# Performance work log

Measured on AMD Instinct MI355X. Metric: run time of the kernel, lower is better.

Reference implementation:

```python
import jax, jax.numpy as jnp
import numpy as np
from jax import lax

# Static config (matches init_kwargs)
DIM = 256; DR = 4; GROUP = 2; NH = 4; KS = 3; NA = 1; NUM_CLASS = 80; MUL = 5.0
CR = DIM // DR            # reduced dim = 64
GC = CR // GROUP          # offset-group channels = 32
HC = CR // NH             # per-head dim = 16
SCALE = HC ** -0.5
B, H, W = 8, 64, 64


def setup_inputs() -> dict:
    key = jax.random.key(0)
    ks_ = jax.random.split(key, 8)
    x = jax.random.normal(ks_[0], (B, DIM, H, W), jnp.float32)
    # offset = absolute pixel coordinates of the base sampling grid
    offset = jax.random.uniform(ks_[1], (B, NA * 2 * KS * KS, H, W), jnp.float32) * (H - 1)
    return dict(
        x=x, offset=offset,
        ln1_g=jnp.ones((DIM,), jnp.float32), ln1_b=jnp.zeros((DIM,), jnp.float32),
        w_qkv=jax.random.normal(ks_[2], (3 * CR, DIM), jnp.float32) * 0.02,
        w_dw=jax.random.normal(ks_[3], (GC, 1, 3, 3), jnp.float32) * 0.1,
        ln2_g=jnp.ones((GC,), jnp.float32), ln2_b=jnp.zeros((GC,), jnp.float32),
        w_off=jax.random.normal(ks_[4], (NA * 2 * KS * KS, GC, 3, 3), jnp.float32) * 0.02,
        b_off=jnp.zeros((NA * 2 * KS * KS,), jnp.float32),
        rpb_table=jax.random.normal(ks_[5], (1, NH, 1, 1, KS * KS, HC), jnp.float32) * 0.02,
        w_proj=jax.random.normal(ks_[6], (DIM, CR), jnp.float32) * 0.02,
        b_proj=jnp.zeros((DIM,), jnp.float32),
        w_cls=jax.random.normal(ks_[7], (NUM_CLASS, DIM), jnp.float32) * 0.02,
        b_cls=jnp.zeros((NUM_CLASS,), jnp.float32),
    )


def _ln_chw(x, g, b, eps=1e-5):
    # LayerNorm over channel dim of NCHW tensor (LayerNormProxy)
    xt = jnp.moveaxis(x, 1, -1)
    m = xt.mean(-1, keepdims=True)
    v = ((xt - m) ** 2).mean(-1, keepdims=True)
    y = (xt - m) * lax.rsqrt(v + eps) * g + b
    return jnp.moveaxis(y, -1, 1)


def _conv(x, w, groups=1, pad=1):
    return lax.conv_general_dilated(x, w, (1, 1), [(pad, pad), (pad, pad)],
                                    feature_group_count=groups,
                                    dimension_numbers=('NCHW', 'OIHW', 'NCHW'))


def _grid_sample(img, grid):
    # img [N,C,H,W]; grid [N,Ho,Wo,2] with (x,y) in [-1,1]; bilinear, zeros pad, align_corners=True
    N, C, Hi, Wi = img.shape
    gx = (grid[..., 0] + 1.0) * 0.5 * (Wi - 1)
    gy = (grid[..., 1] + 1.0) * 0.5 * (Hi - 1)
    x0 = jnp.floor(gx); y0 = jnp.floor(gy)
    x1 = x0 + 1.0;      y1 = y0 + 1.0

    def gather(ix, iy):
        valid = (ix >= 0) & (ix <= Wi - 1) & (iy >= 0) & (iy <= Hi - 1)
        ixc = jnp.clip(ix, 0, Wi - 1).astype(jnp.int32)
        iyc = jnp.clip(iy, 0, Hi - 1).astype(jnp.int32)
        v = jax.vmap(lambda im, yy, xx: im[:, yy, xx])(img, iyc, ixc)  # [N,C,Ho,Wo]
        return v * valid[:, None].astype(img.dtype)

    wa = ((x1 - gx) * (y1 - gy))[:, None]
    wb = ((gx - x0) * (y1 - gy))[:, None]
    wc = ((x1 - gx) * (gy - y0))[:, None]
    wd = ((gx - x0) * (gy - y0))[:, None]
    return (gather(x0, y0) * wa + gather(x1, y0) * wb +
            gather(x0, y1) * wc + gather(x1, y1) * wd)


def _extract_feats(feat, off, Hh, Ww):
    # feat [Bg,GC,H,W]; off [Bg, NA*2*KS*KS, H, W] in pixel coords (row, col)
    Bg = feat.shape[0]
    o = off.reshape(Bg, NA, KS, KS, 2, Hh, Ww)
    o = o.transpose(0, 1, 2, 5, 3, 6, 4)                  # b na kh h kw w d
    o = o.reshape(Bg, NA * KS * Hh, KS * Ww, 2)
    gy = 2.0 * o[..., 0] / (Hh - 1) - 1.0                  # row coord
    gx = 2.0 * o[..., 1] / (Ww - 1) - 1.0                  # col coord
    grid = jnp.stack([gx, gy], -1)                         # flip(-1): (x, y)
    out = _grid_sample(feat, grid)                         # [Bg,GC,NA*KS*H,KS*W]
    out = out.reshape(Bg, GC, NA, KS, Hh, KS, Ww)
    out = out.transpose(0, 2, 3, 5, 1, 4, 6).reshape(Bg, NA * KS * KS, GC, Hh, Ww)
    return out


def reference(x, offset, ln1_g, ln1_b, w_qkv, w_dw, ln2_g, ln2_b, w_off, b_off,
              rpb_table, w_proj, b_proj, w_cls, b_cls):
    Bb, C, Hh, Ww = x.shape
    N = KS * KS

    x_ = _ln_chw(x, ln1_g, ln1_b)
    qkv = jnp.einsum('oc,bchw->bohw', w_qkv, x_)           # [B,3*CR,H,W]
    q, k, v = jnp.split(qkv, 3, axis=1)                    # each [B,CR,H,W]

    # --- offset prediction ---
    q_off = q.reshape(Bb * GROUP, GC, Hh, Ww)
    t = _conv(q_off, w_dw, groups=GC)                      # depthwise 3x3
    t = _ln_chw(t, ln2_g, ln2_b)
    t = jax.nn.gelu(t, approximate=False)
    pred_offset = _conv(t, w_off) + b_off[None, :, None, None]

    off = jnp.broadcast_to(offset[:, None], (Bb, GROUP, NA * 2 * N, Hh, Ww))
    off = off.reshape(Bb * GROUP, NA * 2 * N, Hh, Ww)
    off = jnp.tanh(pred_offset) * MUL + off

    # --- deformable gather of k/v ---
    k = _extract_feats(k.reshape(Bb * GROUP, GC, Hh, Ww), off, Hh, Ww)
    v = _extract_feats(v.reshape(Bb * GROUP, GC, Hh, Ww), off, Hh, Ww)

    def to_heads(t):
        # [(b g), na*n, gc, h, w] -> [b, nh, hw, na, n, hc]
        t = t.reshape(Bb, GROUP, NA, N, GC, Hh, Ww)
        t = t.transpose(0, 5, 6, 2, 3, 1, 4)               # b h w na n g gc
        t = t.reshape(Bb, Hh * Ww, NA, N, NH, HC)
        return t.transpose(0, 4, 1, 2, 3, 5)

    k = to_heads(k) + rpb_table                            # [B,NH,HW,NA,N,HC]
    v = to_heads(v)

    q = q.reshape(Bb, NH, HC, Hh * Ww).transpose(0, 1, 3, 2)  # [B,NH,HW,HC]
    q = jnp.broadcast_to((q * SCALE)[:, :, :, None, :], (Bb, NH, Hh * Ww, NA, HC))

    attn = jnp.einsum('bnpac,bnpakc->bnpak', q, k)         # [B,NH,HW,NA,N]
    attn = jax.nn.softmax(attn, axis=-1)
    out = jnp.einsum('bnpak,bnpakc->bnpac', attn, v)       # [B,NH,HW,NA,HC]

    out = out.transpose(0, 2, 3, 1, 4).reshape(Bb, Hh * Ww, NA, CR)
    out = out @ w_proj.T + b_proj                          # [B,HW,NA,C]
    out = out + x.transpose(0, 2, 3, 1).reshape(Bb, Hh * Ww, 1, C)

    cls = out @ w_cls.T + b_cls                            # [B,HW,NA,NUM_CLASS]
    cls = cls.reshape(Bb, Hh, Ww, NA, NUM_CLASS).transpose(0, 3, 4, 1, 2)
    return cls.reshape(Bb, NA * NUM_CLASS, Hh, Ww)
```

## Files before the change

kernel.cpp:

```cpp
#include <hip/hip_runtime.h>
#include <hip/hip_fp16.h>
#include <math.h>

#define BB   8
#define HW   4096
#define BHW  32768
#define DIM  256
#define CR   64
#define GC   32
#define NHD  4
#define HC   16
#define NTAP 9
#define NCLS 80

#define OFF_QP   0u
#define OFF_QT   2097152u
#define OFF_KT   4194304u
#define OFF_WBF  8388608u
#define OFF_AB   8437760u
#define OFF_T16  8650752u
#define OFF_OFFB 10485760u
#define OFF_AOT  11665408u
#define OFF_WPT  13762560u
#define OFF_WCT  13778944u
#define OFF_WFT  13799424u

typedef short    bf16x8 __attribute__((ext_vector_type(8)));
typedef _Float16 f16x8  __attribute__((ext_vector_type(8)));
typedef float    f32x4  __attribute__((ext_vector_type(4)));

__device__ __forceinline__ unsigned short f2bf(float f) {
    unsigned u = __float_as_uint(f);
    unsigned r = u + 0x7FFFu + ((u >> 16) & 1u);
    return (unsigned short)(r >> 16);
}

__global__ __launch_bounds__(256) void k0_prep(
    const float* __restrict__ wqkv, const float* __restrict__ g1,
    const float* __restrict__ b1, const float* __restrict__ woff,
    const float* __restrict__ wproj, const float* __restrict__ wcls,
    float* __restrict__ ws)
{
    const int t = threadIdx.x;
    const int blk = blockIdx.x;
    if (blk < 192) {
        const int o = blk;
        unsigned short* wbf = (unsigned short*)(ws + OFF_WBF);
        wbf[o * 256 + t] = f2bf(wqkv[o * 256 + t] * g1[t]);
    } else if (blk < 448) {
        const int r = blk - 192;
        unsigned short* wpb = (unsigned short*)(ws + OFF_WPT);
        unsigned short* wcb = (unsigned short*)(ws + OFF_WCT);
        if (t < 64) wpb[r * 64 + t] = f2bf(wproj[r * 64 + t]);
        if (r < 80) wcb[r * 256 + t] = f2bf(wcls[r * 256 + t]);
    } else if (blk < 640) {
        const int o = blk - 448;
        __shared__ float sa[4], sb[4];
        float w = wqkv[o * 256 + t];
        float a = w * g1[t];
        float bb = w * b1[t];
        #pragma unroll
        for (int off = 1; off < 64; off <<= 1) {
            a  += __shfl_xor(a,  off, 64);
            bb += __shfl_xor(bb, off, 64);
        }
        const int wv = t >> 6;
        if ((t & 63) == 0) { sa[wv] = a; sb[wv] = bb; }
        __syncthreads();
        if (t == 0) {
            ws[OFF_AB + o]       = sa[0] + sa[1] + sa[2] + sa[3];
            ws[OFF_AB + 192 + o] = sb[0] + sb[1] + sb[2] + sb[3];
        }
    } else {
        int idx = (blk - 640) * 256 + t;
        if (idx < 2 * 9 * 64 * 8) {
            int j = idx & 7;
            int lane = (idx >> 3) & 63;
            int mw = idx >> 9;
            int m = mw / 9, wo = mw % 9;
            int o = m * 16 + (lane & 15);
            int ic = (lane >> 4) * 8 + j;
            float v = (o < 18) ? woff[(o * 32 + ic) * 9 + wo] : 0.f;
            ((__half*)(ws + OFF_WFT))[idx] = __float2half(v);
        }
    }
}

__global__ __launch_bounds__(512) void k1_mfma(
    const float* __restrict__ x, float* __restrict__ ws)
{
    __shared__ float tile[64 * 193];
    const int t = threadIdx.x;
    const int b = blockIdx.x & 7, row = blockIdx.x >> 3;
    const int wv = __builtin_amdgcn_readfirstlane(t >> 6);
    const int pt = wv & 3, oh = wv >> 2;
    const int lane = t & 63;
    const int quad = lane >> 4, pxl = lane & 15;
    const int colbase = row * 64 + pt * 16 + pxl;
    const unsigned short* wbf = (const unsigned short*)(ws + OFF_WBF);
    const float* AB = ws + OFF_AB;

    f32x4 acc[6];
    #pragma unroll
    for (int ot = 0; ot < 6; ++ot) acc[ot] = (f32x4){0.f, 0.f, 0.f, 0.f};
    float s = 0.f, ss = 0.f;
    const size_t xb0 = (size_t)b * DIM * HW + colbase;

    for (int ks = 0; ks < 8; ++ks) {
        const int cbase = ks * 32 + quad * 8;
        float xv[8];
        #pragma unroll
        for (int j = 0; j < 8; ++j) {
            xv[j] = x[xb0 + (size_t)(cbase + j) * HW];
            s += xv[j]; ss += xv[j] * xv[j];
        }
        union { bf16x8 v; unsigned short u[8]; } bfrag;
        #pragma unroll
        for (int j = 0; j < 8; ++j) bfrag.u[j] = f2bf(xv[j]);
        #pragma unroll
        for (int ot = 0; ot < 6; ++ot) {
            const int orow = (oh * 6 + ot) * 16 + pxl;
            union { float4 f; bf16x8 v; } afrag;
            afrag.f = *(const float4*)&wbf[orow * 256 + cbase];
            acc[ot] = __builtin_amdgcn_mfma_f32_16x16x32_bf16(afrag.v, bfrag.v, acc[ot], 0, 0, 0);
        }
    }

    s  += __shfl_xor(s, 16, 64);  s  += __shfl_xor(s, 32, 64);
    ss += __shfl_xor(ss, 16, 64); ss += __shfl_xor(ss, 32, 64);
    const float m = s * (1.f / 256.f);
    const float rsv = rsqrtf(ss * (1.f / 256.f) - m * m + 1e-5f);

    const int px = pt * 16 + pxl;
    #pragma unroll
    for (int ot = 0; ot < 6; ++ot) {
        #pragma unroll
        for (int r = 0; r < 4; ++r) {
            int o = (oh * 6 + ot) * 16 + quad * 4 + r;
            tile[px * 193 + o] = rsv * (acc[ot][r] - m * AB[o]) + AB[192 + o];
        }
    }
    __syncthreads();

    float*  qp  = ws + OFF_QP;
    __half* qth = (__half*)(ws + OFF_QT);
    __half* kvh = (__half*)(ws + OFF_KT);
    const int colrow = row * 64;
    #pragma unroll
    for (int it = 0; it < 8; ++it) {
        int idx = it * 512 + t;
        int o = idx >> 6, px2 = idx & 63;
        qp[(size_t)(b * 64 + o) * HW + colrow + px2] = tile[px2 * 193 + o];
    }
    #pragma unroll
    for (int it = 0; it < 8; ++it) {
        int idx = it * 512 + t;
        int px2 = idx >> 6, o = idx & 63;
        qth[(size_t)(b * HW + colrow + px2) * 64 + o] = __float2half(tile[px2 * 193 + o]);
    }
    #pragma unroll
    for (int it = 0; it < 4; ++it) {
        int idx = it * 512 + t;
        int px2 = idx >> 5, ch32 = idx & 31;
        int sB = ch32 >> 4, ch = ch32 & 15;
        kvh[(size_t)((2 * b) * HW + colrow + px2) * 64 + sB * 32 + ch]
            = __float2half(tile[px2 * 193 + 64 + ch32]);
    }
    #pragma unroll
    for (int it = 0; it < 4; ++it) {
        int idx = it * 512 + t;
        int px2 = idx >> 5, ch32 = idx & 31;
        int sB = ch32 >> 4, ch = ch32 & 15;
        kvh[(size_t)((2 * b + 1) * HW + colrow + px2) * 64 + sB * 32 + ch]
            = __float2half(tile[px2 * 193 + 96 + ch32]);
    }
    #pragma unroll
    for (int it = 0; it < 4; ++it) {
        int idx = it * 512 + t;
        int px2 = idx >> 5, ch32 = idx & 31;
        int sB = ch32 >> 4, ch = ch32 & 15;
        kvh[(size_t)((2 * b) * HW + colrow + px2) * 64 + sB * 32 + 16 + ch]
            = __float2half(tile[px2 * 193 + 128 + ch32]);
    }
    #pragma unroll
    for (int it = 0; it < 4; ++it) {
        int idx = it * 512 + t;
        int px2 = idx >> 5, ch32 = idx & 31;
        int sB = ch32 >> 4, ch = ch32 & 15;
        kvh[(size_t)((2 * b + 1) * HW + colrow + px2) * 64 + sB * 32 + 16 + ch]
            = __float2half(tile[px2 * 193 + 160 + ch32]);
    }
}

__global__ __launch_bounds__(256) void k2_off_feat(
    const float* __restrict__ wdw, const float* __restrict__ g2, const float* __restrict__ b2,
    float* __restrict__ ws)
{
    __shared__ float qtile[3][32][64];
    __shared__ float rsum[4][64], rsq[4][64], smv[64], srv[64];
    const int t = threadIdx.x;
    const int b = blockIdx.x & 7;
    const int rest = blockIdx.x >> 3;
    const int g = rest & 1;
    const int row = rest >> 1;
    const int bg = b * 2 + g;
    const int p = t & 63;
    const int cq = __builtin_amdgcn_readfirstlane(t >> 6);
    const float* qp = ws + OFF_QP;

    #pragma unroll
    for (int it = 0; it < 6; ++it) {
        int idx = it * 256 + t;
        int rc = idx >> 4;
        int seg = (idx & 15) << 2;
        int dyy = rc >> 5, ch = rc & 31;
        int y = row + dyy - 1;
        float4 v = make_float4(0.f, 0.f, 0.f, 0.f);
        if ((unsigned)y < 64u)
            v = *(const float4*)&qp[(size_t)(b * 64 + g * 32 + ch) * HW + y * 64 + seg];
        *(float4*)&qtile[dyy][ch][seg] = v;
    }
    __syncthreads();

    float vals[8];
    float s = 0.f, ss = 0.f;
    #pragma unroll
    for (int i = 0; i < 8; ++i) {
        int ch = cq * 8 + i;
        float a = 0.f;
        #pragma unroll
        for (int dy = 0; dy < 3; ++dy) {
            #pragma unroll
            for (int dx = 0; dx < 3; ++dx) {
                int xx = p + dx - 1;
                bool vld = (unsigned)xx < 64u;
                float q = qtile[dy][ch][vld ? xx : 0];
                a += (vld ? q : 0.f) * wdw[ch * 9 + dy * 3 + dx];
            }
        }
        vals[i] = a; s += a; ss += a * a;
    }
    rsum[cq][p] = s; rsq[cq][p] = ss;
    __syncthreads();
    if (t < 64) {
        float S = rsum[0][t] + rsum[1][t] + rsum[2][t] + rsum[3][t];
        float Q = rsq[0][t] + rsq[1][t] + rsq[2][t] + rsq[3][t];
        float m = S * (1.f / 32.f);
        float v = Q * (1.f / 32.f) - m * m;
        smv[t] = m; srv[t] = rsqrtf(v + 1e-5f);
    }
    __syncthreads();
    float m = smv[p], rv = srv[p];
    __half* tb16 = (__half*)(ws + OFF_T16);
    #pragma unroll
    for (int i = 0; i < 8; ++i) {
        int ch = cq * 8 + i;
        float u = (vals[i] - m) * rv * g2[ch] + b2[ch];
        vals[i] = 0.5f * u * (1.f + erff(u * 0.70710678118654752f));
    }
    union { float4 f; __half2 h[4]; } o16;
    #pragma unroll
    for (int i = 0; i < 4; ++i) o16.h[i] = __floats2half2_rn(vals[2 * i], vals[2 * i + 1]);
    *(float4*)&tb16[((size_t)bg * HW + row * 64 + p) * 32 + cq * 8] = o16.f;
}

__global__ __launch_bounds__(256) void k3_mfma(
    const float* __restrict__ boff, const float* __restrict__ off_in,
    float* __restrict__ ws)
{
    const int t = threadIdx.x;
    const int b = blockIdx.x & 7;
    const int rest = blockIdx.x >> 3;
    const int g = rest & 1;
    const int rowgrp = (rest >> 1) & 15;
    const int xh = rest >> 5;
    const int wv = __builtin_amdgcn_readfirstlane(t >> 6);
    const int lane = t & 63;
    const int quad = lane >> 4, pxl = lane & 15;
    const int row = rowgrp * 4 + wv;
    const int bg = b * 2 + g;
    const __half* t16 = (const __half*)(ws + OFF_T16);
    const __half* wfA = (const __half*)(ws + OFF_WFT);

    f32x4 acc[2][2];
    #pragma unroll
    for (int i = 0; i < 2; ++i)
        #pragma unroll
        for (int j = 0; j < 2; ++j) acc[i][j] = (f32x4){0.f, 0.f, 0.f, 0.f};

    union FH { float4 f; f16x8 h; };
    #pragma unroll
    for (int wo = 0; wo < 9; ++wo) {
        const int dy = wo / 3, dx = wo % 3;
        const int y = row + dy - 1;
        const bool yv = (unsigned)y < 64u;
        FH a0, a1;
        a0.f = *(const float4*)&wfA[(size_t)((0 * 9 + wo) * 64 + lane) * 8];
        a1.f = *(const float4*)&wfA[(size_t)((1 * 9 + wo) * 64 + lane) * 8];
        #pragma unroll
        for (int tile = 0; tile < 2; ++tile) {
            const int x = xh * 32 + tile * 16 + pxl + dx - 1;
            FH bf;
            bf.f = make_float4(0.f, 0.f, 0.f, 0.f);
            if (yv && (unsigned)x < 64u)
                bf.f = *(const float4*)&t16[((size_t)bg * HW + y * 64 + x) * 32 + quad * 8];
            acc[tile][0] = __builtin_amdgcn_mfma_f32_16x16x32_f16(a0.h, bf.h, acc[tile][0], 0, 0, 0);
            acc[tile][1] = __builtin_amdgcn_mfma_f32_16x16x32_f16(a1.h, bf.h, acc[tile][1], 0, 0, 0);
        }
    }

    float* ob = ws + OFF_OFFB;
    #pragma unroll
    for (int tile = 0; tile < 2; ++tile) {
        const int px = xh * 32 + tile * 16 + pxl;
        #pragma unroll
        for (int mi = 0; mi < 2; ++mi) {
            #pragma unroll
            for (int r = 0; r < 4; ++r) {
                int o = mi * 16 + quad * 4 + r;
                if (o < 18) {
                    float v = acc[tile][mi][r] + boff[o];
                    v = tanhf(v) * 5.0f + off_in[(size_t)(b * 18 + o) * HW + row * 64 + px];
                    ob[(size_t)(bg * 18 + o) * HW + row * 64 + px] = v;
                }
            }
        }
    }
}

__global__ __launch_bounds__(256, 4) void k4_attn(
    const float* __restrict__ rpb, float* __restrict__ ws)
{
    __shared__ float rpb_l[NHD * NTAP * HC];
    for (int i = threadIdx.x; i < NHD * NTAP * HC; i += 256) rpb_l[i] = rpb[i];
    __syncthreads();

    const int t = threadIdx.x;
    const int wave = __builtin_amdgcn_readfirstlane(t >> 6);
    const int g = wave & 1, pxh = wave >> 1;
    const int lane = t & 63;
    const int pxl = lane & 7;
    const int prt = lane >> 3;
    const int s    = prt >> 2;
    const int half = (prt >> 1) & 1;
    const int j    = prt & 1;
    const int b = blockIdx.x & 7;
    const int chunk = blockIdx.x >> 3;
    const int hw = chunk * 16 + pxh * 8 + pxl;
    const int pix = b * HW + hw;
    const int bg = b * 2 + g;
    const int head = g * 2 + s;

    const __half* qth = (const __half*)(ws + OFF_QT);
    const __half* kvh = (const __half*)(ws + OFF_KT);
    const float*  ob  = ws + OFF_OFFB;

    float rr_[NTAP], cc_[NTAP];
    #pragma unroll
    for (int n = 0; n < NTAP; ++n) {
        rr_[n] = ob[(size_t)(bg * 18 + 2 * n) * HW + hw];
        cc_[n] = ob[(size_t)(bg * 18 + 2 * n + 1) * HW + hw];
    }

    union F4H { float4 f; __half2 h[4]; };
    F4H qld;
    qld.f = *(const float4*)&qth[(size_t)pix * 64 + g * 32 + s * 16 + j * 8];
    const float qs = half ? 0.0f : 0.25f;
    float qv[8];
    #pragma unroll
    for (int i = 0; i < 4; ++i) {
        float2 q2 = __half22float2(qld.h[i]);
        qv[2 * i] = q2.x * qs; qv[2 * i + 1] = q2.y * qs;
    }

    const float4* rb4 = (const float4*)(rpb_l + head * (NTAP * HC) + j * 8);
    const __half* kvp = kvh + (size_t)(bg * HW) * 64 + prt * 8;

    __half2 av[NTAP][4];
    float logit[NTAP];

    #pragma unroll
    for (int n = 0; n < NTAP; ++n) {
        float r = rr_[n];
        float c = cc_[n];
        float y0f = floorf(r), x0f = floorf(c);
        float fy = r - y0f, fx = c - x0f;
        int iy0 = (int)y0f, ix0 = (int)x0f;
        float wts[4] = { (1.f - fx) * (1.f - fy), fx * (1.f - fy),
                         (1.f - fx) * fy,         fx * fy };
        __half2 acc0 = __float2half2_rn(0.f), acc1 = acc0, acc2 = acc0, acc3 = acc0;
        #pragma unroll
        for (int corner = 0; corner < 4; ++corner) {
            int cxx = ix0 + (corner & 1);
            int cyy = iy0 + (corner >> 1);
            bool vld = ((unsigned)cxx < 64u) && ((unsigned)cyy < 64u);
            float w = vld ? wts[corner] : 0.f;
            int cxc = min(max(cxx, 0), 63);
            int cyc = min(max(cyy, 0), 63);
            F4H kv;
            kv.f = *(const float4*)&kvp[(size_t)(cyc * 64 + cxc) * 64];
            __half2 w2 = __float2half2_rn(w);
            acc0 = __hfma2(kv.h[0], w2, acc0);
            acc1 = __hfma2(kv.h[1], w2, acc1);
            acc2 = __hfma2(kv.h[2], w2, acc2);
            acc3 = __hfma2(kv.h[3], w2, acc3);
        }
        av[n][0] = acc0; av[n][1] = acc1; av[n][2] = acc2; av[n][3] = acc3;
        float4 r0 = rb4[n * 4], r1 = rb4[n * 4 + 1];
        float2 a0 = __half22float2(acc0), a1 = __half22float2(acc1);
        float2 a2 = __half22float2(acc2), a3 = __half22float2(acc3);
        float part = qv[0] * (a0.x + r0.x) + qv[1] * (a0.y + r0.y)
                   + qv[2] * (a1.x + r0.z) + qv[3] * (a1.y + r0.w)
                   + qv[4] * (a2.x + r1.x) + qv[5] * (a2.y + r1.y)
                   + qv[6] * (a3.x + r1.z) + qv[7] * (a3.y + r1.w);
        part += __shfl_xor(part, 8, 64);
        part += __shfl_xor(part, 16, 64);
        logit[n] = part;
    }

    float m = logit[0];
    #pragma unroll
    for (int n = 1; n < NTAP; ++n) m = fmaxf(m, logit[n]);
    float l = 0.f;
    #pragma unroll
    for (int n = 0; n < NTAP; ++n) { logit[n] = __expf(logit[n] - m); l += logit[n]; }
    const float inv = 1.f / l;

    __half2 o0 = __float2half2_rn(0.f), o1 = o0, o2 = o0, o3 = o0;
    #pragma unroll
    for (int n = 0; n < NTAP; ++n) {
        __half2 p2 = __float2half2_rn(logit[n]);
        o0 = __hfma2(av[n][0], p2, o0);
        o1 = __hfma2(av[n][1], p2, o1);
        o2 = __hfma2(av[n][2], p2, o2);
        o3 = __hfma2(av[n][3], p2, o3);
    }
    if (half) {
        unsigned short* aob = (unsigned short*)(ws + OFF_AOT);
        const int cb = head * 16 + j * 8;
        float2 f0 = __half22float2(o0), f1 = __half22float2(o1);
        float2 f2 = __half22float2(o2), f3 = __half22float2(o3);
        union { float4 f; unsigned short u[8]; } pk;
        pk.u[0] = f2bf(f0.x * inv); pk.u[1] = f2bf(f0.y * inv);
        pk.u[2] = f2bf(f1.x * inv); pk.u[3] = f2bf(f1.y * inv);
        pk.u[4] = f2bf(f2.x * inv); pk.u[5] = f2bf(f2.y * inv);
        pk.u[6] = f2bf(f3.x * inv); pk.u[7] = f2bf(f3.y * inv);
        *(float4*)&aob[(size_t)pix * 64 + cb] = pk.f;
    }
}

__global__ __launch_bounds__(256) void k5_mfma(
    const float* __restrict__ x, const float* __restrict__ bproj,
    const float* __restrict__ bcls, float* __restrict__ ws, float* __restrict__ out)
{
    __shared__ unsigned short tmp[64][264];
    const int t = threadIdx.x;
    const int b = blockIdx.x & 7, row = blockIdx.x >> 3;
    const int wv = __builtin_amdgcn_readfirstlane(t >> 6);
    const int lane = t & 63, quad = lane >> 4, pxl = lane & 15;
    const int px = wv * 16 + pxl;
    const int pixcol = row * 64 + px;
    const size_t pix = (size_t)b * HW + pixcol;
    const unsigned short* aob = (const unsigned short*)(ws + OFF_AOT);
    const unsigned short* wpb = (const unsigned short*)(ws + OFF_WPT);
    const unsigned short* wcb = (const unsigned short*)(ws + OFF_WCT);

    union FB { float4 f; bf16x8 v; };
    FB bf0, bf1;
    bf0.f = *(const float4*)&aob[pix * 64 + quad * 8];
    bf1.f = *(const float4*)&aob[pix * 64 + 32 + quad * 8];

    #pragma unroll 4
    for (int ot = 0; ot < 16; ++ot) {
        f32x4 acc = (f32x4){0.f, 0.f, 0.f, 0.f};
        FB a0, a1;
        const int om = ot * 16 + pxl;
        a0.f = *(const float4*)&wpb[om * 64 + quad * 8];
        a1.f = *(const float4*)&wpb[om * 64 + 32 + quad * 8];
        acc = __builtin_amdgcn_mfma_f32_16x16x32_bf16(a0.v, bf0.v, acc, 0, 0, 0);
        acc = __builtin_amdgcn_mfma_f32_16x16x32_bf16(a1.v, bf1.v, acc, 0, 0, 0);
        union { unsigned short u[4]; ushort2 s2[2]; } pk;
        #pragma unroll
        for (int r = 0; r < 4; ++r) {
            int o = ot * 16 + quad * 4 + r;
            float v = acc[r] + bproj[o] + x[(size_t)(b * DIM + o) * HW + pixcol];
            pk.u[r] = f2bf(v);
        }
        *(ushort4*)&tmp[px][ot * 16 + quad * 4] = *(ushort4*)pk.u;
    }
    __syncthreads();

    f32x4 acc2[5];
    #pragma unroll
    for (int oc = 0; oc < 5; ++oc) acc2[oc] = (f32x4){0.f, 0.f, 0.f, 0.f};
    #pragma unroll
    for (int kc = 0; kc < 8; ++kc) {
        FB bb;
        bb.f = *(const float4*)&tmp[px][kc * 32 + quad * 8];
        #pragma unroll
        for (int oc = 0; oc < 5; ++oc) {
            FB aa;
            aa.f = *(const float4*)&wcb[(oc * 16 + pxl) * 256 + kc * 32 + quad * 8];
            acc2[oc] = __builtin_amdgcn_mfma_f32_16x16x32_bf16(aa.v, bb.v, acc2[oc], 0, 0, 0);
        }
    }
    #pragma unroll
    for (int oc = 0; oc < 5; ++oc) {
        #pragma unroll
        for (int r = 0; r < 4; ++r) {
            int o = oc * 16 + quad * 4 + r;
            out[(size_t)(b * NCLS + o) * HW + pixcol] = acc2[oc][r] + bcls[o];
        }
    }
}

extern "C" void kernel_launch(void* const* d_in, const int* in_sizes, int n_in,
                              void* d_out, int out_size, void* d_ws, size_t ws_size,
                              hipStream_t stream)
{
    const float* x     = (const float*)d_in[0];
    const float* off   = (const float*)d_in[1];
    const float* g1    = (const float*)d_in[2];
    const float* b1    = (const float*)d_in[3];
    const float* wqkv  = (const float*)d_in[4];
    const float* wdw   = (const float*)d_in[5];
    const float* g2    = (const float*)d_in[6];
    const float* b2    = (const float*)d_in[7];
    const float* woff  = (const float*)d_in[8];
    const float* boff  = (const float*)d_in[9];
    const float* rpb   = (const float*)d_in[10];
    const float* wproj = (const float*)d_in[11];
    const float* bproj = (const float*)d_in[12];
    const float* wcls  = (const float*)d_in[13];
    const float* bcls  = (const float*)d_in[14];
    float* ws  = (float*)d_ws;
    float* out = (float*)d_out;

    hipLaunchKernelGGL(k0_prep,     dim3(676),  dim3(256), 0, stream, wqkv, g1, b1, woff, wproj, wcls, ws);
    hipLaunchKernelGGL(k1_mfma,     dim3(512),  dim3(512), 0, stream, x, ws);
    hipLaunchKernelGGL(k2_off_feat, dim3(1024), dim3(256), 0, stream, wdw, g2, b2, ws);
    hipLaunchKernelGGL(k3_mfma,     dim3(512),  dim3(256), 0, stream, boff, off, ws);
    hipLaunchKernelGGL(k4_attn,     dim3(2048), dim3(256), 0, stream, rpb, ws);
    hipLaunchKernelGGL(k5_mfma,     dim3(512),  dim3(256), 0, stream, x, bproj, bcls, ws, out);
}
```

Before: 218.7 us.

## Fuse attention output with projection and classifier GEMMs in one kernel

Merges the attention kernel with the projection plus classifier MFMA kernel. Each 16-pixel block keeps its bf16 attention output in shared memory and applies both GEMMs there. This removes a global write and re-read of the attention output and one kernel launch. In exchange, each block reloads the projection and classifier weights for only 16 pixels instead of 64, and the classifier stage uses just 5 tiles over 4 waves, so one wave does double work.

```diff
diff --git a/kernel.cpp b/kernel.cpp
--- a/kernel.cpp
+++ b/kernel.cpp
@@ -20,7 +20,6 @@
 #define OFF_AB   8437760u
 #define OFF_T16  8650752u
 #define OFF_OFFB 10485760u
-#define OFF_AOT  11665408u
 #define OFF_WPT  13762560u
 #define OFF_WCT  13778944u
 #define OFF_WFT  13799424u
@@ -328,10 +327,14 @@
     }
 }
 
-__global__ __launch_bounds__(256, 4) void k4_attn(
-    const float* __restrict__ rpb, float* __restrict__ ws)
+__global__ __launch_bounds__(256, 4) void k45_attn_proj(
+    const float* __restrict__ rpb, const float* __restrict__ x,
+    const float* __restrict__ bproj, const float* __restrict__ bcls,
+    float* __restrict__ ws, float* __restrict__ out)
 {
     __shared__ float rpb_l[NHD * NTAP * HC];
+    __shared__ unsigned short ao_l[16][72];
+    __shared__ unsigned short tmp[16][264];
     for (int i = threadIdx.x; i < NHD * NTAP * HC; i += 256) rpb_l[i] = rpb[i];
     __syncthreads();
 
@@ -346,7 +349,8 @@
     const int j    = prt & 1;
     const int b = blockIdx.x & 7;
     const int chunk = blockIdx.x >> 3;
-    const int hw = chunk * 16 + pxh * 8 + pxl;
+    const int hw_base = chunk * 16;
+    const int hw = hw_base + pxh * 8 + pxl;
     const int pix = b * HW + hw;
     const int bg = b * 2 + g;
     const int head = g * 2 + s;
@@ -436,7 +440,6 @@
         o3 = __hfma2(av[n][3], p2, o3);
     }
     if (half) {
-        unsigned short* aob = (unsigned short*)(ws + OFF_AOT);
         const int cb = head * 16 + j * 8;
         float2 f0 = __half22float2(o0), f1 = __half22float2(o1);
         float2 f2 = __half22float2(o2), f3 = __half22float2(o3);
@@ -445,71 +448,54 @@
         pk.u[2] = f2bf(f1.x * inv); pk.u[3] = f2bf(f1.y * inv);
         pk.u[4] = f2bf(f2.x * inv); pk.u[5] = f2bf(f2.y * inv);
         pk.u[6] = f2bf(f3.x * inv); pk.u[7] = f2bf(f3.y * inv);
-        *(float4*)&aob[(size_t)pix * 64 + cb] = pk.f;
-    }
-}
-
-__global__ __launch_bounds__(256) void k5_mfma(
-    const float* __restrict__ x, const float* __restrict__ bproj,
-    const float* __restrict__ bcls, float* __restrict__ ws, float* __restrict__ out)
-{
-    __shared__ unsigned short tmp[64][264];
-    const int t = threadIdx.x;
-    const int b = blockIdx.x & 7, row = blockIdx.x >> 3;
-    const int wv = __builtin_amdgcn_readfirstlane(t >> 6);
-    const int lane = t & 63, quad = lane >> 4, pxl = lane & 15;
-    const int px = wv * 16 + pxl;
-    const int pixcol = row * 64 + px;
-    const size_t pix = (size_t)b * HW + pixcol;
-    const unsigned short* aob = (const unsigned short*)(ws + OFF_AOT);
+        *(float4*)&ao_l[pxh * 8 + pxl][cb] = pk.f;
+    }
+    __syncthreads();
+
+    const int q4  = lane >> 4;
+    const int p16 = lane & 15;
     const unsigned short* wpb = (const unsigned short*)(ws + OFF_WPT);
     const unsigned short* wcb = (const unsigned short*)(ws + OFF_WCT);
 
     union FB { float4 f; bf16x8 v; };
     FB bf0, bf1;
-    bf0.f = *(const float4*)&aob[pix * 64 + quad * 8];
-    bf1.f = *(const float4*)&aob[pix * 64 + 32 + quad * 8];
-
-    #pragma unroll 4
-    for (int ot = 0; ot < 16; ++ot) {
+    bf0.f = *(const float4*)&ao_l[p16][q4 * 8];
+    bf1.f = *(const float4*)&ao_l[p16][32 + q4 * 8];
+
+    #pragma unroll
+    for (int ot = wave * 4; ot < wave * 4 + 4; ++ot) {
         f32x4 acc = (f32x4){0.f, 0.f, 0.f, 0.f};
         FB a0, a1;
-        const int om = ot * 16 + pxl;
-        a0.f = *(const float4*)&wpb[om * 64 + quad * 8];
-        a1.f = *(const float4*)&wpb[om * 64 + 32 + quad * 8];
+        const int om = ot * 16 + p16;
+        a0.f = *(const float4*)&wpb[om * 64 + q4 * 8];
+        a1.f = *(const float4*)&wpb[om * 64 + 32 + q4 * 8];
         acc = __builtin_amdgcn_mfma_f32_16x16x32_bf16(a0.v, bf0.v, acc, 0, 0, 0);
         acc = __builtin_amdgcn_mfma_f32_16x16x32_bf16(a1.v, bf1.v, acc, 0, 0, 0);
-        union { unsigned short u[4]; ushort2 s2[2]; } pk;
+        union { unsigned short u[4]; } pk;
         #pragma unroll
         for (int r = 0; r < 4; ++r) {
-            int o = ot * 16 + quad * 4 + r;
-            float v = acc[r] + bproj[o] + x[(size_t)(b * DIM + o) * HW + pixcol];
+            int o = ot * 16 + q4 * 4 + r;
+            float v = acc[r] + bproj[o] + x[(size_t)(b * DIM + o) * HW + hw_base + p16];
             pk.u[r] = f2bf(v);
         }
-        *(ushort4*)&tmp[px][ot * 16 + quad * 4] = *(ushort4*)pk.u;
-    }
-    __syncthreads();
-
-    f32x4 acc2[5];
-    #pragma unroll
-    for (int oc = 0; oc < 5; ++oc) acc2[oc] = (f32x4){0.f, 0.f, 0.f, 0.f};
-    #pragma unroll
-    for (int kc = 0; kc < 8; ++kc) {
-        FB bb;
-        bb.f = *(const float4*)&tmp[px][kc * 32 + quad * 8];
-        #pragma unroll
-        for (int oc = 0; oc < 5; ++oc) {
-            FB aa;
-            aa.f = *(const float4*)&wcb[(oc * 16 + pxl) * 256 + kc * 32 + quad * 8];
-            acc2[oc] = __builtin_amdgcn_mfma_f32_16x16x32_bf16(aa.v, bb.v, acc2[oc], 0, 0, 0);
-        }
-    }
-    #pragma unroll
-    for (int oc = 0; oc < 5; ++oc) {
+        *(ushort4*)&tmp[p16][ot * 16 + q4 * 4] = *(ushort4*)pk.u;
+    }
+    __syncthreads();
+
+    #pragma unroll
+    for (int oc = wave; oc < 5; oc += 4) {
+        f32x4 acc2 = (f32x4){0.f, 0.f, 0.f, 0.f};
+        #pragma unroll
+        for (int kc = 0; kc < 8; ++kc) {
+            FB bb, aa;
+            bb.f = *(const float4*)&tmp[p16][kc * 32 + q4 * 8];
+            aa.f = *(const float4*)&wcb[(oc * 16 + p16) * 256 + kc * 32 + q4 * 8];
+            acc2 = __builtin_amdgcn_mfma_f32_16x16x32_bf16(aa.v, bb.v, acc2, 0, 0, 0);
+        }
         #pragma unroll
         for (int r = 0; r < 4; ++r) {
-            int o = oc * 16 + quad * 4 + r;
-            out[(size_t)(b * NCLS + o) * HW + pixcol] = acc2[oc][r] + bcls[o];
+            int o = oc * 16 + q4 * 4 + r;
+            out[(size_t)(b * NCLS + o) * HW + hw_base + p16] = acc2[r] + bcls[o];
         }
     }
 }
@@ -536,10 +522,9 @@
     float* ws  = (float*)d_ws;
     float* out = (float*)d_out;
 
-    hipLaunchKernelGGL(k0_prep,     dim3(676),  dim3(256), 0, stream, wqkv, g1, b1, woff, wproj, wcls, ws);
-    hipLaunchKernelGGL(k1_mfma,     dim3(512),  dim3(512), 0, stream, x, ws);
-    hipLaunchKernelGGL(k2_off_feat, dim3(1024), dim3(256), 0, stream, wdw, g2, b2, ws);
-    hipLaunchKernelGGL(k3_mfma,     dim3(512),  dim3(256), 0, stream, boff, off, ws);
-    hipLaunchKernelGGL(k4_attn,     dim3(2048), dim3(256), 0, stream, rpb, ws);
-    hipLaunchKernelGGL(k5_mfma,     dim3(512),  dim3(256), 0, stream, x, bproj, bcls, ws, out);
-}
+    hipLaunchKernelGGL(k0_prep,       dim3(676),  dim3(256), 0, stream, wqkv, g1, b1, woff, wproj, wcls, ws);
+    hipLaunchKernelGGL(k1_mfma,       dim3(512),  dim3(512), 0, stream, x, ws);
+    hipLaunchKernelGGL(k2_off_feat,   dim3(1024), dim3(256), 0, stream, wdw, g2, b2, ws);
+    hipLaunchKernelGGL(k3_mfma,       dim3(512),  dim3(256), 0, stream, boff, off, ws);
+    hipLaunchKernelGGL(k45_attn_proj, dim3(2048), dim3(256), 0, stream, rpb, x, bproj, bcls, ws, out);
+}
```

New measurement: 200.7 us. 8.2% less time.
